# Optimization experiments

Measured on AMD Instinct MI355X. Metric: run time of the kernel, lower is better.

The kernel has to match this reference:

```python
import jax, jax.numpy as jnp
import numpy as np


def _ste_round(r):
    # straight-through round
    return r + jax.lax.stop_gradient(jnp.round(r) - r)


def quant_sym(x, s, qn, qp):
    # symmetric LSQ-style fake-quant: clamp(round(x/s)) * s
    r = jnp.clip(x / s, qn, qp)
    return _ste_round(r) * s


def quant_asym(x, s, beta, qn, qp):
    # asymmetric fake-quant with learnable zero-point beta
    r = jnp.clip((x - beta) / s, qn, qp)
    return _ste_round(r) * s + beta


def quant_weight_statsq(w, n_bits=8):
    # statsq: per-output-channel scale from weight statistics
    qp = 2 ** (n_bits - 1) - 1          # 127
    qn = -(2 ** (n_bits - 1))           # -128
    s = 2.0 * jnp.mean(jnp.abs(w), axis=1, keepdims=True) / jnp.sqrt(float(qp))
    return quant_sym(w, s, qn, qp)


def setup_inputs() -> dict:
    key = jax.random.key(0)
    ks = jax.random.split(key, 8)
    B, N, C, H = 4, 4096, 1024, 4096
    x = jax.random.normal(ks[0], (B, N, C), dtype=jnp.float32)
    w1 = jax.random.normal(ks[1], (H, C), dtype=jnp.float32) * (1.0 / np.sqrt(C))
    b1 = jax.random.normal(ks[2], (H,), dtype=jnp.float32) * 0.01
    w2 = jax.random.normal(ks[3], (C, H), dtype=jnp.float32) * (1.0 / np.sqrt(H))
    b2 = jax.random.normal(ks[4], (C,), dtype=jnp.float32) * 0.01
    # learnable LSQ activation scales (per input channel), kept positive
    s_a1 = 0.05 + 0.05 * jax.random.uniform(ks[5], (C,), dtype=jnp.float32)
    s_a2 = 0.02 + 0.02 * jax.random.uniform(ks[6], (H,), dtype=jnp.float32)
    beta2 = jnp.zeros((H,), dtype=jnp.float32)
    return {"x": x, "w1": w1, "b1": b1, "w2": w2, "b2": b2,
            "s_a1": s_a1, "s_a2": s_a2, "beta2": beta2}


def reference(x, w1, b1, w2, b2, s_a1, s_a2, beta2):
    # fc1: symmetric 8-bit LSQ on input, statsq 8-bit on weight
    xq = quant_sym(x, s_a1, -128, 127)
    wq1 = quant_weight_statsq(w1)
    h = jnp.einsum('bnc,hc->bnh', xq, wq1) + b1
    h = jax.nn.gelu(h, approximate=False)  # nn.GELU default (exact erf)
    # drop1 = identity in eval
    # fc2: asymmetric 8-bit LSQ on (non-negative-skewed) activations
    hq = quant_asym(h, s_a2, beta2, 0, 255)
    wq2 = quant_weight_statsq(w2)
    out = jnp.einsum('bnh,ch->bnc', hq, wq2) + b2
    # drop2 = identity in eval
    return out
```

## Files before the change

### kernel.cpp

```cpp
#include <hip/hip_runtime.h>
#include <cstdint>
#include <cstddef>

typedef __attribute__((ext_vector_type(8))) short short8;
typedef __attribute__((ext_vector_type(4))) float f32x4;
typedef __attribute__((ext_vector_type(4))) unsigned short ushort4_t;

__device__ __forceinline__ unsigned short f2bf(float f) {
  unsigned u = __float_as_uint(f);
  u += 0x7FFFu + ((u >> 16) & 1u);
  return (unsigned short)(u >> 16);
}

__device__ __forceinline__ void gload_lds16(const void* g, void* lds) {
  __builtin_amdgcn_global_load_lds((const __attribute__((address_space(1))) void*)g,
                                   (__attribute__((address_space(3))) void*)lds,
                                   16, 0, 0);
}

__device__ __forceinline__ float erf_fast(float v) {
  float x = fabsf(v);
  float t = __builtin_amdgcn_rcpf(fmaf(0.3275911f, x, 1.0f));
  float p = fmaf(1.061405429f, t, -1.453152027f);
  p = fmaf(p, t, 1.421413741f);
  p = fmaf(p, t, -0.284496736f);
  p = fmaf(p, t, 0.254829592f);
  p = p * t;
  float e = fmaf(-p, __expf(-x * x), 1.0f);
  unsigned s = __float_as_uint(v) & 0x80000000u;
  return __uint_as_float(__float_as_uint(e) | s);
}

__global__ void quant_x_kernel(const float4* __restrict__ x, const float* __restrict__ s_a1,
                               ushort4_t* __restrict__ xq, int n4, int c4mask) {
  const int stride = gridDim.x * blockDim.x;
  for (int i = blockIdx.x * blockDim.x + threadIdx.x; i < n4; i += stride) {
    float4 v = x[i];
    int c = (i & c4mask) << 2;
    float vv[4] = {v.x, v.y, v.z, v.w};
    ushort4_t o;
#pragma unroll
    for (int j = 0; j < 4; ++j) {
      float s = s_a1[c + j];
      float r = vv[j] / s;
      r = fminf(fmaxf(r, -128.f), 127.f);
      o[j] = f2bf(rintf(r) * s);
    }
    xq[i] = o;
  }
}

__global__ void quant_w_kernel(const float* __restrict__ w, unsigned short* __restrict__ wq,
                               int cols) {
  const int row = blockIdx.x;
  const float* wr = w + (size_t)row * cols;
  float part = 0.f;
  for (int j = threadIdx.x; j < cols; j += blockDim.x) part += fabsf(wr[j]);
#pragma unroll
  for (int o = 32; o > 0; o >>= 1) part += __shfl_down(part, o, 64);
  __shared__ float wsum[4];
  if ((threadIdx.x & 63) == 0) wsum[threadIdx.x >> 6] = part;
  __syncthreads();
  float mean = (wsum[0] + wsum[1] + wsum[2] + wsum[3]) / (float)cols;
  float s = 2.f * mean / sqrtf(127.f);
  unsigned short* wqr = wq + (size_t)row * cols;
  for (int j = threadIdx.x; j < cols; j += blockDim.x) {
    float r = wr[j] / s;
    r = fminf(fmaxf(r, -128.f), 127.f);
    wqr[j] = f2bf(rintf(r) * s);
  }
}

#define BAR() __builtin_amdgcn_s_barrier()
#define LGKM0() { asm volatile("s_waitcnt lgkmcnt(0)" ::: "memory"); __builtin_amdgcn_sched_barrier(0); }

#define STG(gbase, ldsbuf, h, kt) { \
  _Pragma("unroll") for (int i_ = 0; i_ < 2; ++i_) { \
    const int rb_ = (h) * 128 + (w * 2 + i_) * 8; \
    gload_lds16((gbase) + (size_t)rb_ * K + (size_t)(kt) * 64, (void*)((ldsbuf) + rb_ * 64)); } }

#define LDA_(dst, buf, mh) { \
  _Pragma("unroll") for (int mi_ = 0; mi_ < 4; ++mi_) { \
    dst[mi_][0] = *(const short8*)((buf) + aBase + (mh) * 4096 + mi_ * 1024 + ck0); \
    dst[mi_][1] = *(const short8*)((buf) + aBase + (mh) * 4096 + mi_ * 1024 + ck1); } }

#define LDB_(dst, buf, nh) { \
  _Pragma("unroll") for (int ni_ = 0; ni_ < 2; ++ni_) { \
    dst[ni_][0] = *(const short8*)((buf) + bBase + (nh) * 2048 + ni_ * 1024 + ck0); \
    dst[ni_][1] = *(const short8*)((buf) + bBase + (nh) * 2048 + ni_ * 1024 + ck1); } }

#define MMQ(aR, bR, mh, nh) { \
  _Pragma("unroll") for (int kk_ = 0; kk_ < 2; ++kk_) \
  _Pragma("unroll") for (int mi_ = 0; mi_ < 4; ++mi_) \
  _Pragma("unroll") for (int ni_ = 0; ni_ < 2; ++ni_) \
    acc[(mh) * 4 + mi_][(nh) * 2 + ni_] = __builtin_amdgcn_mfma_f32_16x16x32_bf16( \
        aR[mi_][kk_], bR[ni_][kk_], acc[(mh) * 4 + mi_][(nh) * 2 + ni_], 0, 0, 0); }

template <int EPI>
__global__ __launch_bounds__(512, 2) void gemm_bt_8ph(
    const unsigned short* __restrict__ A, const unsigned short* __restrict__ B,
    const float* __restrict__ bias, const float* __restrict__ s2,
    const float* __restrict__ beta, unsigned short* __restrict__ Cq,
    float* __restrict__ Cf, int N, int K)
{
  __shared__ __align__(16) unsigned short As0[256 * 64];
  __shared__ __align__(16) unsigned short As1[256 * 64];
  __shared__ __align__(16) unsigned short Bs0[256 * 64];
  __shared__ __align__(16) unsigned short Bs1[256 * 64];

  const int tid = threadIdx.x;
  const int w = tid >> 6, ll = tid & 63;
  const int wr = w >> 2, wc = w & 3;
  const long bm = (long)blockIdx.x * 256;
  const long bn = (long)blockIdx.y * 256;

  const int srow = ll >> 3;
  const int scol = ((ll & 7) ^ srow) << 3;
  const unsigned short* Agl = A + ((size_t)bm + srow) * K + scol;
  const unsigned short* Bgl = B + ((size_t)bn + srow) * K + scol;

  const int lhi = ll >> 4, llo = ll & 15, l7 = ll & 7;
  const int ck0 = ((0 * 4 + lhi) ^ l7) * 8;
  const int ck1 = ((1 * 4 + lhi) ^ l7) * 8;
  const int aBase = (wr * 128 + llo) * 64;
  const int bBase = (wc * 64 + llo) * 64;

  f32x4 acc[8][4] = {};
  short8 a0[4][2], a1[4][2], b0[2][2], b1[2][2];

  const int nkt = K >> 6;

  STG(Agl, As0, 0, 0); STG(Agl, As0, 1, 0);
  STG(Bgl, Bs0, 0, 0); STG(Bgl, Bs0, 1, 0);
  if (nkt > 1) { STG(Agl, As1, 0, 1); STG(Agl, As1, 1, 1); STG(Bgl, Bs1, 0, 1); }
  if (nkt > 1) { asm volatile("s_waitcnt vmcnt(6)" ::: "memory"); }
  else         { asm volatile("s_waitcnt vmcnt(0)" ::: "memory"); }
  __builtin_amdgcn_sched_barrier(0);
  BAR();

  for (int t = 0; t < nkt; ++t) {
    unsigned short* Asb = (t & 1) ? As1 : As0;
    unsigned short* Bsb = (t & 1) ? Bs1 : Bs0;
    unsigned short* Bsn = (t & 1) ? Bs0 : Bs1;
    const bool i1 = (t + 1 < nkt), i2 = (t + 2 < nkt);

    LDA_(a0, Asb, 0);
    LDB_(b0, Bsb, 0);
    if (i1) STG(Bgl, Bsn, 1, t + 1);
    BAR(); LGKM0();
    __builtin_amdgcn_s_setprio(1); MMQ(a0, b0, 0, 0); __builtin_amdgcn_s_setprio(0);
    BAR();

    LDA_(a1, Asb, 1);
    if (i2) STG(Agl, Asb, 0, t + 2);
    BAR(); LGKM0();
    __builtin_amdgcn_s_setprio(1); MMQ(a1, b0, 1, 0); __builtin_amdgcn_s_setprio(0);
    BAR();

    LDB_(b1, Bsb, 1);
    if (i2) STG(Agl, Asb, 1, t + 2);
    BAR(); LGKM0();
    __builtin_amdgcn_s_setprio(1); MMQ(a1, b1, 1, 1); __builtin_amdgcn_s_setprio(0);
    BAR();

    if (i2) STG(Bgl, Bsb, 0, t + 2);
    BAR();
    __builtin_amdgcn_s_setprio(1); MMQ(a0, b1, 0, 1); __builtin_amdgcn_s_setprio(0);
    if (i2)      { asm volatile("s_waitcnt vmcnt(6)" ::: "memory"); }
    else if (i1) { asm volatile("s_waitcnt vmcnt(0)" ::: "memory"); }
    __builtin_amdgcn_sched_barrier(0);
    BAR();
  }

  const int lr = lhi;
  const int lc = llo;
#pragma unroll
  for (int NI = 0; NI < 4; ++NI) {
    const long col = bn + wc * 64 + NI * 16 + lc;
    const float bv = bias[col];
    float sv = 1.f, bev = 0.f, inv = 1.f;
    if (EPI == 0) { sv = s2[col]; bev = beta[col]; inv = 1.0f / sv; }
#pragma unroll
    for (int MI = 0; MI < 8; ++MI) {
#pragma unroll
      for (int r = 0; r < 4; ++r) {
        const size_t rowg = (size_t)(bm + wr * 128 + MI * 16 + lr * 4 + r);
        float v = acc[MI][NI][r] + bv;
        if (EPI == 0) {
          float g = 0.5f * v * (1.f + erf_fast(v * 0.70710678118654752f));
          float rr = (g - bev) * inv;
          rr = fminf(fmaxf(rr, 0.f), 255.f);
          Cq[rowg * N + col] = f2bf(fmaf(rintf(rr), sv, bev));
        } else {
          Cf[rowg * N + col] = v;
        }
      }
    }
  }
}

extern "C" void kernel_launch(void* const* d_in, const int* in_sizes, int n_in,
                              void* d_out, int out_size, void* d_ws, size_t ws_size,
                              hipStream_t stream) {
  const float* x     = (const float*)d_in[0];
  const float* w1    = (const float*)d_in[1];
  const float* b1    = (const float*)d_in[2];
  const float* w2    = (const float*)d_in[3];
  const float* b2    = (const float*)d_in[4];
  const float* s_a1  = (const float*)d_in[5];
  const float* s_a2  = (const float*)d_in[6];
  const float* beta2 = (const float*)d_in[7];
  float* out = (float*)d_out;

  const int C = 1024, H = 4096;
  const int M = in_sizes[0] / C;

  unsigned short* xq  = (unsigned short*)d_ws;
  unsigned short* wq1 = xq  + (size_t)M * C;
  unsigned short* wq2 = wq1 + (size_t)H * C;
  unsigned short* hq  = wq2 + (size_t)C * H;

  quant_x_kernel<<<2048, 256, 0, stream>>>((const float4*)x, s_a1, (ushort4_t*)xq,
                                           M * C / 4, C / 4 - 1);
  quant_w_kernel<<<H, 256, 0, stream>>>(w1, wq1, C);
  quant_w_kernel<<<C, 256, 0, stream>>>(w2, wq2, H);

  dim3 g1(M / 256, H / 256);
  gemm_bt_8ph<0><<<g1, 512, 0, stream>>>(xq, wq1, b1, s_a2, beta2, hq, nullptr, H, C);
  dim3 g2(M / 256, C / 256);
  gemm_bt_8ph<1><<<g2, 512, 0, stream>>>(hq, wq2, b2, nullptr, nullptr, nullptr, out, C, H);
}
```

Baseline: 379.5 us.

## Restructure GEMM main loop to a single barrier per K-tile with register prefetch

Replaces the four-phase main loop, which had several barriers and full LDS waits per K-tile, with a loop that has one barrier per tile. All global-to-LDS loads for tile t+2 are issued together after the barrier. The first A/B register fragments for the next tile are read from LDS before the last MFMA quadrant, so those reads overlap compute. Partial lgkmcnt waits let MFMAs start while later fragments are still arriving. The cost is more live registers and a full vmcnt(0) wait each iteration, and the loop now assumes at least two K-tiles.

```diff
diff --git a/kernel.cpp b/kernel.cpp
--- a/kernel.cpp
+++ b/kernel.cpp
@@ -72,7 +72,11 @@
 }
 
 #define BAR() __builtin_amdgcn_s_barrier()
-#define LGKM0() { asm volatile("s_waitcnt lgkmcnt(0)" ::: "memory"); __builtin_amdgcn_sched_barrier(0); }
+#define SB() __builtin_amdgcn_sched_barrier(0)
+#define LGKM(n) { asm volatile("s_waitcnt lgkmcnt(" #n ")" ::: "memory"); SB(); }
+#define VMC0() { asm volatile("s_waitcnt vmcnt(0)" ::: "memory"); SB(); }
+#define PRIO1() __builtin_amdgcn_s_setprio(1)
+#define PRIO0() __builtin_amdgcn_s_setprio(0)
 
 #define STG(gbase, ldsbuf, h, kt) { \
   _Pragma("unroll") for (int i_ = 0; i_ < 2; ++i_) { \
@@ -97,7 +101,7 @@
         aR[mi_][kk_], bR[ni_][kk_], acc[(mh) * 4 + mi_][(nh) * 2 + ni_], 0, 0, 0); }
 
 template <int EPI>
-__global__ __launch_bounds__(512, 2) void gemm_bt_8ph(
+__global__ __launch_bounds__(512, 2) void gemm_bt_pl(
     const unsigned short* __restrict__ A, const unsigned short* __restrict__ B,
     const float* __restrict__ bias, const float* __restrict__ s2,
     const float* __restrict__ beta, unsigned short* __restrict__ Cq,
@@ -132,44 +136,39 @@
 
   STG(Agl, As0, 0, 0); STG(Agl, As0, 1, 0);
   STG(Bgl, Bs0, 0, 0); STG(Bgl, Bs0, 1, 0);
-  if (nkt > 1) { STG(Agl, As1, 0, 1); STG(Agl, As1, 1, 1); STG(Bgl, Bs1, 0, 1); }
-  if (nkt > 1) { asm volatile("s_waitcnt vmcnt(6)" ::: "memory"); }
-  else         { asm volatile("s_waitcnt vmcnt(0)" ::: "memory"); }
-  __builtin_amdgcn_sched_barrier(0);
+  STG(Agl, As1, 0, 1); STG(Agl, As1, 1, 1);
+  STG(Bgl, Bs1, 0, 1); STG(Bgl, Bs1, 1, 1);
+  asm volatile("s_waitcnt vmcnt(8)" ::: "memory"); SB();
   BAR();
+  LDA_(a0, As0, 0);
+  LDB_(b0, Bs0, 0);
 
   for (int t = 0; t < nkt; ++t) {
     unsigned short* Asb = (t & 1) ? As1 : As0;
     unsigned short* Bsb = (t & 1) ? Bs1 : Bs0;
+    unsigned short* Asn = (t & 1) ? As0 : As1;
     unsigned short* Bsn = (t & 1) ? Bs0 : Bs1;
     const bool i1 = (t + 1 < nkt), i2 = (t + 2 < nkt);
 
-    LDA_(a0, Asb, 0);
-    LDB_(b0, Bsb, 0);
-    if (i1) STG(Bgl, Bsn, 1, t + 1);
-    BAR(); LGKM0();
-    __builtin_amdgcn_s_setprio(1); MMQ(a0, b0, 0, 0); __builtin_amdgcn_s_setprio(0);
+    LDB_(b1, Bsb, 1);
+    LGKM(4);
+    PRIO1(); MMQ(a0, b0, 0, 0); PRIO0();
+    LDA_(a1, Asb, 1);
+    LGKM(8);
+    PRIO1(); MMQ(a0, b1, 0, 1); PRIO0();
+    LGKM(0);
+    PRIO1(); MMQ(a1, b0, 1, 0); PRIO0();
+    VMC0();
     BAR();
-
-    LDA_(a1, Asb, 1);
-    if (i2) STG(Agl, Asb, 0, t + 2);
-    BAR(); LGKM0();
-    __builtin_amdgcn_s_setprio(1); MMQ(a1, b0, 1, 0); __builtin_amdgcn_s_setprio(0);
-    BAR();
-
-    LDB_(b1, Bsb, 1);
-    if (i2) STG(Agl, Asb, 1, t + 2);
-    BAR(); LGKM0();
-    __builtin_amdgcn_s_setprio(1); MMQ(a1, b1, 1, 1); __builtin_amdgcn_s_setprio(0);
-    BAR();
-
-    if (i2) STG(Bgl, Bsb, 0, t + 2);
-    BAR();
-    __builtin_amdgcn_s_setprio(1); MMQ(a0, b1, 0, 1); __builtin_amdgcn_s_setprio(0);
-    if (i2)      { asm volatile("s_waitcnt vmcnt(6)" ::: "memory"); }
-    else if (i1) { asm volatile("s_waitcnt vmcnt(0)" ::: "memory"); }
-    __builtin_amdgcn_sched_barrier(0);
-    BAR();
+    if (i2) {
+      STG(Agl, Asb, 0, t + 2); STG(Agl, Asb, 1, t + 2);
+      STG(Bgl, Bsb, 0, t + 2); STG(Bgl, Bsb, 1, t + 2);
+    }
+    if (i1) {
+      LDA_(a0, Asn, 0);
+      LDB_(b0, Bsn, 0);
+    }
+    PRIO1(); MMQ(a1, b1, 1, 1); PRIO0();
   }
 
   const int lr = lhi;
@@ -226,7 +225,7 @@
   quant_w_kernel<<<C, 256, 0, stream>>>(w2, wq2, H);
 
   dim3 g1(M / 256, H / 256);
-  gemm_bt_8ph<0><<<g1, 512, 0, stream>>>(xq, wq1, b1, s_a2, beta2, hq, nullptr, H, C);
+  gemm_bt_pl<0><<<g1, 512, 0, stream>>>(xq, wq1, b1, s_a2, beta2, hq, nullptr, H, C);
   dim3 g2(M / 256, C / 256);
-  gemm_bt_8ph<1><<<g2, 512, 0, stream>>>(hq, wq2, b2, nullptr, nullptr, nullptr, out, C, H);
-}
+  gemm_bt_pl<1><<<g2, 512, 0, stream>>>(hq, wq2, b2, nullptr, nullptr, nullptr, out, C, H);
+}
```

Result: faster. 367.0 us (-3.3%).
